# Optimization experiments

Measured on AMD Instinct MI355X. Metric: run time of the kernel, lower is better.

## Reference

```python
import jax, jax.numpy as jnp
import numpy as np

N = 50000   # residue nodes
E = 800000  # edges per edge type
T = 3       # edge types
L = 3       # conv layers (len(hidden_channels)-1)
IN, H, ENC, OUT, K = 64, 128, 100, 32, 128
COMMIT = 0.25
EPS = 1e-5


def gelu(x):
    return jax.nn.gelu(x, approximate=False)  # torch nn.GELU default (erf)


def setup_inputs() -> dict:
    key = jax.random.key(0)
    ks = iter(jax.random.split(key, 40))
    p = lambda shp, s=0.05: jax.random.normal(next(ks), shp, jnp.float32) * s
    inp = {
        'x_res': p((N, IN), 1.0),
        'x_AA': p((N, 20), 1.0),
        'edge_index': jax.random.randint(next(ks), (T, 2, E), 0, N, jnp.int32),
        # input block
        'ln_gamma': jnp.ones((IN,), jnp.float32),
        'ln_beta': jnp.zeros((IN,), jnp.float32),
        'W1': p((IN, 2 * H)), 'b1': jnp.zeros((2 * H,), jnp.float32),
        'W2': p((2 * H, H)), 'b2': jnp.zeros((H,), jnp.float32),
        # body: SAGE convs, [layer, edge_type, ...]
        'sage_Wl': p((L, T, H, H)),  # applied to aggregated neighbors
        'sage_Wr': p((L, T, H, H)),  # applied to root
        'sage_b': jnp.zeros((L, T, H), jnp.float32),
        # GraphNorm per layer
        'gn_weight': jnp.ones((L, H), jnp.float32),
        'gn_bias': jnp.zeros((L, H), jnp.float32),
        'gn_scale': jnp.ones((L, H), jnp.float32),  # mean_scale
        # head
        'Wh1': p((H * L, ENC)), 'bh1': jnp.zeros((ENC,), jnp.float32),
        'Wh2': p((ENC, ENC)), 'bh2': jnp.zeros((ENC,), jnp.float32),
        'Wo1': p((ENC + 20, ENC)), 'bo1': jnp.zeros((ENC,), jnp.float32),
        'Wo2': p((ENC, ENC)), 'bo2': jnp.zeros((ENC,), jnp.float32),
        'Wo3': p((ENC, OUT)), 'bo3': jnp.zeros((OUT,), jnp.float32),
        # VQ codebook
        'codebook': p((K, OUT), 0.5),
    }
    return inp


def _sage(x, src, dst, Wl, Wr, b):
    # SAGEConv, mean aggregation: out = Wl @ mean_{src->dst}(x[src]) + Wr @ x + b
    msg = x[src]                                             # [E, H] gather
    s = jax.ops.segment_sum(msg, dst, num_segments=N)        # [N, H] scatter-add
    cnt = jax.ops.segment_sum(jnp.ones((msg.shape[0],), x.dtype), dst, num_segments=N)
    agg = s / jnp.maximum(cnt, 1.0)[:, None]
    return agg @ Wl + x @ Wr + b


def _graphnorm(x, weight, bias, scale):
    # PyG GraphNorm over a single graph
    out = x - scale * x.mean(0)
    var = (out * out).mean(0)
    return out * jax.lax.rsqrt(var + EPS) * weight + bias


def reference(x_res, x_AA, edge_index, ln_gamma, ln_beta, W1, b1, W2, b2,
              sage_Wl, sage_Wr, sage_b, gn_weight, gn_bias, gn_scale,
              Wh1, bh1, Wh2, bh2, Wo1, bo1, Wo2, bo2, Wo3, bo3, codebook):
    # input: LayerNorm + (dropout = identity in eval) + inmlp
    mu = x_res.mean(-1, keepdims=True)
    var = x_res.var(-1, keepdims=True)
    xr = (x_res - mu) * jax.lax.rsqrt(var + EPS) * ln_gamma + ln_beta
    x = gelu(gelu(xr @ W1 + b1) @ W2 + b2)                   # [N, H]

    # body: per-edge-type SAGE conv -> stack-mean -> GELU -> GraphNorm; JK cat
    x_save = []
    for i in range(L):
        xs = [_sage(x, edge_index[t, 0], edge_index[t, 1],
                    sage_Wl[i, t], sage_Wr[i, t], sage_b[i, t]) for t in range(T)]
        x = jnp.mean(jnp.stack(xs, 0), 0)
        x = gelu(x)
        x = _graphnorm(x, gn_weight[i], gn_bias[i], gn_scale[i])
        x_save.append(x)
    x = jnp.concatenate(x_save, axis=1)                      # [N, H*L] JumpingKnowledge cat

    # head
    x = gelu(gelu(x @ Wh1 + bh1) @ Wh2 + bh2)
    x = jnp.concatenate([x, x_AA], axis=1)
    x = gelu(x @ Wo1 + bo1)
    x = gelu(x @ Wo2 + bo2)
    x = jnp.tanh(x @ Wo3 + bo3)                              # [N, OUT]

    # VectorQuantizer (straight-through)
    d = (jnp.sum(x * x, 1, keepdims=True)
         - 2.0 * x @ codebook.T
         + jnp.sum(codebook * codebook, 1)[None, :])         # [N, K]
    idx = jnp.argmin(d, axis=1)
    q = codebook[idx]                                        # [N, OUT]
    e_latent = jnp.mean((jax.lax.stop_gradient(q) - x) ** 2)
    q_latent = jnp.mean((q - jax.lax.stop_gradient(x)) ** 2)
    vq_loss = q_latent + COMMIT * e_latent
    z_q = x + jax.lax.stop_gradient(q - x)
    return z_q, vq_loss
```

## Files before the change

kernel.cpp:

```cpp
#include <hip/hip_runtime.h>

#define N_ 50000
#define E_ 800000
#define T_ 3
#define NG_ (T_ * N_)
#define EPS_ 1e-5f

__device__ __forceinline__ float gelu_f(float x) {
    return 0.5f * x * (1.0f + erff(x * 0.70710678118654752440f));
}

__global__ void k_prep(const float* __restrict__ Wl, const float* __restrict__ Wr,
                       const float* __restrict__ b, float* wls, float* wra, float* ba) {
    int i = blockIdx.x * 256 + threadIdx.x;
    const float third = 1.0f / 3.0f;
    if (i < 9 * 128 * 128) wls[i] = Wl[i] * third;
    if (i < 3 * 128 * 128) {
        int l = i >> 14, rem = i & 16383;
        const float* p = Wr + l * 3 * 16384 + rem;
        wra[i] = (p[0] + p[16384] + p[32768]) * third;
    }
    if (i < 3 * 128) {
        int l = i >> 7, c = i & 127;
        const float* p = b + l * 3 * 128 + c;
        ba[i] = (p[0] + p[128] + p[256]) * third;
    }
}

__global__ void k_link(const int* __restrict__ EI, int* __restrict__ head, int* __restrict__ nxt) {
    int i = blockIdx.x * 256 + threadIdx.x;
    if (i >= T_ * E_) return;
    int t = i / E_, e = i - t * E_;
    int d = EI[(t * 2 + 1) * E_ + e];
    nxt[i] = atomicExch(&head[t * N_ + d], i);
}

__global__ __launch_bounds__(256) void k_compact(
    const int* __restrict__ EI, const int* __restrict__ head, const int* __restrict__ nxt,
    int* __restrict__ cursor, int* __restrict__ cnt, int* __restrict__ rpA,
    float* __restrict__ inv, int* __restrict__ csr) {
    int tid = threadIdx.x;
    int g = blockIdx.x * 256 + tid;
    bool ok = (g < NG_);
    int lane = tid & 63;
    int c = 0;
    int h = -1;
    if (ok) {
        h = head[g];
        int e = h;
        while (e >= 0) { c++; e = nxt[e]; }
        cnt[g] = c;
        inv[g] = 1.0f / (float)(c > 0 ? c : 1);
    }
    int x = c;
    for (int off = 1; off < 64; off <<= 1) {
        int y = __shfl_up(x, off);
        if (lane >= off) x += y;
    }
    int total = __shfl(x, 63);
    int base = 0;
    if (lane == 63 && total > 0) base = atomicAdd(cursor, total);
    base = __shfl(base, 63);
    if (ok) {
        int pos = base + x - c;
        rpA[g] = pos;
        int e = h;
        while (e >= 0) {
            int t = e / E_, idx = e - t * E_;
            csr[pos++] = EI[(t * 2) * E_ + idx];
            e = nxt[e];
        }
    }
}

__global__ __launch_bounds__(256) void k_inmlp(
    const float* __restrict__ xres, const float* __restrict__ gam, const float* __restrict__ bet,
    const float* __restrict__ W1, const float* __restrict__ b1,
    const float* __restrict__ W2, const float* __restrict__ b2, float* __restrict__ x0) {
    __shared__ float xr[32][68];
    __shared__ float h1[32][260];
    int tid = threadIdx.x;
    int base = blockIdx.x * 32;
    for (int i = 0; i < 2; ++i) {
        int f4 = i * 256 + tid;
        int r = f4 >> 4, c4 = f4 & 15;
        float4 v = make_float4(0.f, 0.f, 0.f, 0.f);
        int gr = base + r;
        if (gr < N_) v = *(const float4*)&xres[gr * 64 + c4 * 4];
        *(float4*)&xr[r][c4 * 4] = v;
    }
    __syncthreads();
    if (tid < 32) {
        int r = tid;
        float s = 0.f;
        for (int k = 0; k < 64; ++k) s += xr[r][k];
        float mu = s * (1.0f / 64.0f);
        float v = 0.f;
        for (int k = 0; k < 64; ++k) { float d = xr[r][k] - mu; v += d * d; }
        float rs = rsqrtf(v * (1.0f / 64.0f) + EPS_);
        for (int k = 0; k < 64; ++k)
            xr[r][k] = (xr[r][k] - mu) * rs * gam[k] + bet[k];
    }
    __syncthreads();
    {
        int tx = tid & 63, ty = tid >> 6;
        int c0 = tx * 4, r0 = ty * 8;
        float acc[8][4];
        for (int r = 0; r < 8; ++r)
            for (int j = 0; j < 4; ++j) acc[r][j] = b1[c0 + j];
        for (int k0 = 0; k0 < 64; k0 += 4) {
            float4 a[8], w[4];
            for (int r = 0; r < 8; ++r) a[r] = *(const float4*)&xr[r0 + r][k0];
            for (int kk = 0; kk < 4; ++kk) w[kk] = *(const float4*)&W1[(k0 + kk) * 256 + c0];
            for (int kk = 0; kk < 4; ++kk)
                for (int r = 0; r < 8; ++r) {
                    float as = (&a[r].x)[kk];
                    acc[r][0] = fmaf(as, w[kk].x, acc[r][0]);
                    acc[r][1] = fmaf(as, w[kk].y, acc[r][1]);
                    acc[r][2] = fmaf(as, w[kk].z, acc[r][2]);
                    acc[r][3] = fmaf(as, w[kk].w, acc[r][3]);
                }
        }
        for (int r = 0; r < 8; ++r)
            for (int j = 0; j < 4; ++j) h1[r0 + r][c0 + j] = gelu_f(acc[r][j]);
    }
    __syncthreads();
    {
        int tx = tid & 31, ty = tid >> 5;
        int c0 = tx * 4, r0 = ty * 4;
        float acc[4][4];
        for (int r = 0; r < 4; ++r)
            for (int j = 0; j < 4; ++j) acc[r][j] = b2[c0 + j];
        for (int k0 = 0; k0 < 256; k0 += 4) {
            float4 a[4], w[4];
            for (int r = 0; r < 4; ++r) a[r] = *(const float4*)&h1[r0 + r][k0];
            for (int kk = 0; kk < 4; ++kk) w[kk] = *(const float4*)&W2[(k0 + kk) * 128 + c0];
            for (int kk = 0; kk < 4; ++kk)
                for (int r = 0; r < 4; ++r) {
                    float as = (&a[r].x)[kk];
                    acc[r][0] = fmaf(as, w[kk].x, acc[r][0]);
                    acc[r][1] = fmaf(as, w[kk].y, acc[r][1]);
                    acc[r][2] = fmaf(as, w[kk].z, acc[r][2]);
                    acc[r][3] = fmaf(as, w[kk].w, acc[r][3]);
                }
        }
        for (int r = 0; r < 4; ++r) {
            int gr = base + r0 + r;
            if (gr < N_) {
                float4 v = make_float4(gelu_f(acc[r][0]), gelu_f(acc[r][1]),
                                       gelu_f(acc[r][2]), gelu_f(acc[r][3]));
                *(float4*)&x0[(long)gr * 128 + c0] = v;
            }
        }
    }
}

__global__ __launch_bounds__(256) void k_gather(
    const int* __restrict__ rpA, const int* __restrict__ cnt, const int* __restrict__ csr,
    const float* __restrict__ inv, const float* __restrict__ X, int ldx, float* __restrict__ agg) {
    int tid = threadIdx.x;
    int g = blockIdx.x * 4 + (tid >> 6);
    if (g >= NG_) return;
    int lane = tid & 63;
    int sub = lane >> 4;
    int f = (lane & 15) * 8;
    int start = rpA[g];
    int end = start + cnt[g];
    float4 s0 = make_float4(0.f, 0.f, 0.f, 0.f);
    float4 s1 = make_float4(0.f, 0.f, 0.f, 0.f);
    for (int e = start + sub; e < end; e += 4) {
        int sn = csr[e];
        const float* row = &X[(long)sn * ldx + f];
        const float4 v0 = *(const float4*)row;
        const float4 v1 = *(const float4*)(row + 4);
        s0.x += v0.x; s0.y += v0.y; s0.z += v0.z; s0.w += v0.w;
        s1.x += v1.x; s1.y += v1.y; s1.z += v1.z; s1.w += v1.w;
    }
    s0.x += __shfl_xor(s0.x, 16); s0.y += __shfl_xor(s0.y, 16);
    s0.z += __shfl_xor(s0.z, 16); s0.w += __shfl_xor(s0.w, 16);
    s1.x += __shfl_xor(s1.x, 16); s1.y += __shfl_xor(s1.y, 16);
    s1.z += __shfl_xor(s1.z, 16); s1.w += __shfl_xor(s1.w, 16);
    s0.x += __shfl_xor(s0.x, 32); s0.y += __shfl_xor(s0.y, 32);
    s0.z += __shfl_xor(s0.z, 32); s0.w += __shfl_xor(s0.w, 32);
    s1.x += __shfl_xor(s1.x, 32); s1.y += __shfl_xor(s1.y, 32);
    s1.z += __shfl_xor(s1.z, 32); s1.w += __shfl_xor(s1.w, 32);
    if (sub == 0) {
        float iv = inv[g];
        float* op = &agg[(long)g * 128 + f];
        *(float4*)op = make_float4(s0.x * iv, s0.y * iv, s0.z * iv, s0.w * iv);
        *(float4*)(op + 4) = make_float4(s1.x * iv, s1.y * iv, s1.z * iv, s1.w * iv);
    }
}

__global__ __launch_bounds__(256) void k_gemm_body(
    const float* __restrict__ X, int ldx, const float* __restrict__ agg,
    const float* __restrict__ wls_l, const float* __restrict__ wra_l, const float* __restrict__ ba_l,
    float* __restrict__ g_out, float* __restrict__ cs_l) {
    __shared__ float xs[64][132];
    __shared__ float sd[8][128];
    int tid = threadIdx.x;
    int base = blockIdx.x * 64;
    int tx = tid & 31, ty = tid >> 5;
    int c0 = tx * 4, r0 = ty * 8;
    float acc[8][4];
    for (int r = 0; r < 8; ++r)
        for (int j = 0; j < 4; ++j) acc[r][j] = ba_l[c0 + j];
    for (int seg = 0; seg < 4; ++seg) {
        const float* src; long ld;
        if (seg < 3) { src = agg + ((long)seg * N_ + base) * 128; ld = 128; }
        else         { src = X + (long)base * ldx; ld = ldx; }
        __syncthreads();
        for (int i = 0; i < 8; ++i) {
            int f4 = i * 256 + tid;
            int r = f4 >> 5, c4 = f4 & 31;
            float4 v = make_float4(0.f, 0.f, 0.f, 0.f);
            if (base + r < N_) v = *(const float4*)&src[(long)r * ld + c4 * 4];
            *(float4*)&xs[r][c4 * 4] = v;
        }
        __syncthreads();
        const float* W = (seg < 3) ? (wls_l + seg * 16384) : wra_l;
        for (int k0 = 0; k0 < 128; k0 += 4) {
            float4 a[8], w[4];
            for (int r = 0; r < 8; ++r) a[r] = *(const float4*)&xs[r0 + r][k0];
            for (int kk = 0; kk < 4; ++kk) w[kk] = *(const float4*)&W[(k0 + kk) * 128 + c0];
            for (int kk = 0; kk < 4; ++kk)
                for (int r = 0; r < 8; ++r) {
                    float as = (&a[r].x)[kk];
                    acc[r][0] = fmaf(as, w[kk].x, acc[r][0]);
                    acc[r][1] = fmaf(as, w[kk].y, acc[r][1]);
                    acc[r][2] = fmaf(as, w[kk].z, acc[r][2]);
                    acc[r][3] = fmaf(as, w[kk].w, acc[r][3]);
                }
        }
    }
    float csum[4] = {0.f, 0.f, 0.f, 0.f};
    for (int r = 0; r < 8; ++r) {
        int gr = base + r0 + r;
        if (gr < N_) {
            float g0 = gelu_f(acc[r][0]), g1 = gelu_f(acc[r][1]);
            float g2 = gelu_f(acc[r][2]), g3 = gelu_f(acc[r][3]);
            *(float4*)&g_out[(long)gr * 128 + c0] = make_float4(g0, g1, g2, g3);
            csum[0] += g0; csum[1] += g1; csum[2] += g2; csum[3] += g3;
        }
    }
    *(float4*)&sd[ty][c0] = make_float4(csum[0], csum[1], csum[2], csum[3]);
    __syncthreads();
    if (tid < 128) {
        float t = 0.f;
        for (int i = 0; i < 8; ++i) t += sd[i][tid];
        atomicAdd(&cs_l[tid], t);
    }
}

__global__ __launch_bounds__(256) void k_pass2(const float* __restrict__ g,
                                               const float* __restrict__ cs_l,
                                               const float* __restrict__ gsc, float* __restrict__ cq_l) {
    __shared__ float sd[256];
    int tid = threadIdx.x;
    int c = tid & 127, half = tid >> 7;
    int base = blockIdx.x * 128 + half * 64;
    float sm = gsc[c] * (cs_l[c] / 50000.0f);
    float s = 0.f;
    for (int i = 0; i < 64; ++i) {
        int r = base + i;
        if (r < N_) { float o = g[(long)r * 128 + c] - sm; s += o * o; }
    }
    sd[tid] = s;
    __syncthreads();
    if (tid < 128) atomicAdd(&cq_l[c], sd[tid] + sd[tid + 128]);
}
__global__ __launch_bounds__(256) void k_pass3(const float* __restrict__ g,
                                               const float* __restrict__ cs_l, const float* __restrict__ cq_l,
                                               const float* __restrict__ gsc,
                                               const float* __restrict__ gw, const float* __restrict__ gb,
                                               float* __restrict__ xs_l) {
    int tid = threadIdx.x;
    int c = tid & 127, half = tid >> 7;
    int base = blockIdx.x * 128 + half * 64;
    float sm = gsc[c] * (cs_l[c] / 50000.0f);
    float var = cq_l[c] / 50000.0f;
    float mul = rsqrtf(var + EPS_) * gw[c];
    float add = gb[c];
    for (int i = 0; i < 64; ++i) {
        int r = base + i;
        if (r < N_) xs_l[(long)r * 384 + c] = (g[(long)r * 128 + c] - sm) * mul + add;
    }
}

__global__ __launch_bounds__(256) void k_head1(const float* __restrict__ xsave,
    const float* __restrict__ Wh1, const float* __restrict__ bh1,
    const float* __restrict__ Wh2, const float* __restrict__ bh2,
    float* __restrict__ h2out) {
    __shared__ float at[64][68];
    __shared__ float h1b[64][104];
    int tid = threadIdx.x;
    int base = blockIdx.x * 64;
    int tx = tid & 31, ty = tid >> 5;
    int c0 = tx * 4, r0 = ty * 8;
    bool valid = (c0 < 100);
    float acc[8][4];
    for (int r = 0; r < 8; ++r)
        for (int j = 0; j < 4; ++j) acc[r][j] = valid ? bh1[c0 + j] : 0.f;
    for (int kt = 0; kt < 6; ++kt) {
        __syncthreads();
        for (int i = 0; i < 4; ++i) {
            int f4 = i * 256 + tid;
            int r = f4 >> 4, c4 = f4 & 15;
            float4 v = make_float4(0.f, 0.f, 0.f, 0.f);
            int gr = base + r;
            if (gr < N_) v = *(const float4*)&xsave[(long)gr * 384 + kt * 64 + c4 * 4];
            *(float4*)&at[r][c4 * 4] = v;
        }
        __syncthreads();
        if (valid) {
            for (int k0 = 0; k0 < 64; k0 += 4) {
                float4 a[8], w[4];
                for (int r = 0; r < 8; ++r) a[r] = *(const float4*)&at[r0 + r][k0];
                for (int kk = 0; kk < 4; ++kk) w[kk] = *(const float4*)&Wh1[(kt * 64 + k0 + kk) * 100 + c0];
                for (int kk = 0; kk < 4; ++kk)
                    for (int r = 0; r < 8; ++r) {
                        float as = (&a[r].x)[kk];
                        acc[r][0] = fmaf(as, w[kk].x, acc[r][0]);
                        acc[r][1] = fmaf(as, w[kk].y, acc[r][1]);
                        acc[r][2] = fmaf(as, w[kk].z, acc[r][2]);
                        acc[r][3] = fmaf(as, w[kk].w, acc[r][3]);
                    }
            }
        }
    }
    __syncthreads();
    if (valid)
        for (int r = 0; r < 8; ++r)
            for (int j = 0; j < 4; ++j) h1b[r0 + r][c0 + j] = gelu_f(acc[r][j]);
    __syncthreads();
    {
        float acc2[8][4];
        for (int r = 0; r < 8; ++r)
            for (int j = 0; j < 4; ++j) acc2[r][j] = valid ? bh2[c0 + j] : 0.f;
        if (valid) {
            for (int k0 = 0; k0 < 100; k0 += 4) {
                float4 a[8], w[4];
                for (int r = 0; r < 8; ++r) a[r] = *(const float4*)&h1b[r0 + r][k0];
                for (int kk = 0; kk < 4; ++kk) w[kk] = *(const float4*)&Wh2[(k0 + kk) * 100 + c0];
                for (int kk = 0; kk < 4; ++kk)
                    for (int r = 0; r < 8; ++r) {
                        float as = (&a[r].x)[kk];
                        acc2[r][0] = fmaf(as, w[kk].x, acc2[r][0]);
                        acc2[r][1] = fmaf(as, w[kk].y, acc2[r][1]);
                        acc2[r][2] = fmaf(as, w[kk].z, acc2[r][2]);
                        acc2[r][3] = fmaf(as, w[kk].w, acc2[r][3]);
                    }
            }
            for (int r = 0; r < 8; ++r) {
                int gr = base + r0 + r;
                if (gr < N_) {
                    float4 v = make_float4(gelu_f(acc2[r][0]), gelu_f(acc2[r][1]),
                                           gelu_f(acc2[r][2]), gelu_f(acc2[r][3]));
                    *(float4*)&h2out[(long)gr * 100 + c0] = v;
                }
            }
        }
    }
}

__global__ __launch_bounds__(128) void k_head2(const float* __restrict__ h2,
    const float* __restrict__ xAA,
    const float* __restrict__ Wo1, const float* __restrict__ bo1,
    const float* __restrict__ Wo2, const float* __restrict__ bo2,
    const float* __restrict__ Wo3, const float* __restrict__ bo3,
    const float* __restrict__ cb, float* __restrict__ zq, float* __restrict__ loss) {
    __shared__ __align__(16) float smem[13216];
    float* A  = smem;
    float* B  = smem + 3968;
    float* XF = smem + 7296;
    float* CB = smem + 8448;
    float* CC = smem + 13056;
    float* SR = smem + 13184;
    int tid = threadIdx.x;
    int base = blockIdx.x * 32;
    for (int i = 0; i < 8; ++i) {
        int f4 = i * 128 + tid;
        int k = f4 >> 3, j4 = f4 & 7;
        float4 v = *(const float4*)&cb[k * 32 + j4 * 4];
        *(float4*)&CB[k * 36 + j4 * 4] = v;
    }
    for (int i = 0; i < 7; ++i) {
        int f4 = i * 128 + tid;
        if (f4 < 800) {
            int r = f4 / 25, c4 = f4 - r * 25;
            float4 v = make_float4(0.f, 0.f, 0.f, 0.f);
            int gr = base + r;
            if (gr < N_) v = *(const float4*)&h2[(long)gr * 100 + c4 * 4];
            *(float4*)&A[r * 124 + c4 * 4] = v;
        }
    }
    for (int i = 0; i < 2; ++i) {
        int f4 = i * 128 + tid;
        if (f4 < 160) {
            int r = f4 / 5, c4 = f4 - r * 5;
            float4 v = make_float4(0.f, 0.f, 0.f, 0.f);
            int gr = base + r;
            if (gr < N_) v = *(const float4*)&xAA[(long)gr * 20 + c4 * 4];
            *(float4*)&A[r * 124 + 100 + c4 * 4] = v;
        }
    }
    __syncthreads();
    if (tid < 128) {
        float s = 0.f;
        for (int j = 0; j < 32; ++j) { float v = CB[tid * 36 + j]; s += v * v; }
        CC[tid] = s;
    }
    int tx = tid & 31, ty = tid >> 5;
    int c0 = tx * 4, r0 = ty * 8;
    bool valid = (c0 < 100);
    {
        float acc[8][4];
        for (int r = 0; r < 8; ++r)
            for (int j = 0; j < 4; ++j) acc[r][j] = valid ? bo1[c0 + j] : 0.f;
        if (valid) {
            for (int k0 = 0; k0 < 120; k0 += 4) {
                float4 a[8], w[4];
                for (int r = 0; r < 8; ++r) a[r] = *(const float4*)&A[(r0 + r) * 124 + k0];
                for (int kk = 0; kk < 4; ++kk) w[kk] = *(const float4*)&Wo1[(k0 + kk) * 100 + c0];
                for (int kk = 0; kk < 4; ++kk)
                    for (int r = 0; r < 8; ++r) {
                        float as = (&a[r].x)[kk];
                        acc[r][0] = fmaf(as, w[kk].x, acc[r][0]);
                        acc[r][1] = fmaf(as, w[kk].y, acc[r][1]);
                        acc[r][2] = fmaf(as, w[kk].z, acc[r][2]);
                        acc[r][3] = fmaf(as, w[kk].w, acc[r][3]);
                    }
            }
        }
        __syncthreads();
        if (valid)
            for (int r = 0; r < 8; ++r)
                for (int j = 0; j < 4; ++j) B[(r0 + r) * 104 + c0 + j] = gelu_f(acc[r][j]);
    }
    __syncthreads();
    {
        float acc[8][4];
        for (int r = 0; r < 8; ++r)
            for (int j = 0; j < 4; ++j) acc[r][j] = valid ? bo2[c0 + j] : 0.f;
        if (valid) {
            for (int k0 = 0; k0 < 100; k0 += 4) {
                float4 a[8], w[4];
                for (int r = 0; r < 8; ++r) a[r] = *(const float4*)&B[(r0 + r) * 104 + k0];
                for (int kk = 0; kk < 4; ++kk) w[kk] = *(const float4*)&Wo2[(k0 + kk) * 100 + c0];
                for (int kk = 0; kk < 4; ++kk)
                    for (int r = 0; r < 8; ++r) {
                        float as = (&a[r].x)[kk];
                        acc[r][0] = fmaf(as, w[kk].x, acc[r][0]);
                        acc[r][1] = fmaf(as, w[kk].y, acc[r][1]);
                        acc[r][2] = fmaf(as, w[kk].z, acc[r][2]);
                        acc[r][3] = fmaf(as, w[kk].w, acc[r][3]);
                    }
            }
        }
        __syncthreads();
        if (valid)
            for (int r = 0; r < 8; ++r)
                for (int j = 0; j < 4; ++j) A[(r0 + r) * 124 + c0 + j] = gelu_f(acc[r][j]);
    }
    __syncthreads();
    {
        int c0b = (tid & 7) * 4, rg = tid >> 3;
        int r0b = rg * 2;
        float acc[2][4];
        for (int r = 0; r < 2; ++r)
            for (int j = 0; j < 4; ++j) acc[r][j] = bo3[c0b + j];
        for (int k0 = 0; k0 < 100; k0 += 4) {
            float4 a[2], w[4];
            for (int r = 0; r < 2; ++r) a[r] = *(const float4*)&A[(r0b + r) * 124 + k0];
            for (int kk = 0; kk < 4; ++kk) w[kk] = *(const float4*)&Wo3[(k0 + kk) * 32 + c0b];
            for (int kk = 0; kk < 4; ++kk)
                for (int r = 0; r < 2; ++r) {
                    float as = (&a[r].x)[kk];
                    acc[r][0] = fmaf(as, w[kk].x, acc[r][0]);
                    acc[r][1] = fmaf(as, w[kk].y, acc[r][1]);
                    acc[r][2] = fmaf(as, w[kk].z, acc[r][2]);
                    acc[r][3] = fmaf(as, w[kk].w, acc[r][3]);
                }
        }
        for (int r = 0; r < 2; ++r)
            for (int j = 0; j < 4; ++j) XF[(r0b + r) * 36 + c0b + j] = tanhf(acc[r][j]);
    }
    __syncthreads();
    {
        int node = tid >> 2, t4 = tid & 3;
        float4 xv[8];
        for (int j4 = 0; j4 < 8; ++j4) xv[j4] = *(const float4*)&XF[node * 36 + j4 * 4];
        float xx = 0.f;
        for (int j4 = 0; j4 < 8; ++j4)
            xx += xv[j4].x * xv[j4].x + xv[j4].y * xv[j4].y + xv[j4].z * xv[j4].z + xv[j4].w * xv[j4].w;
        float best = 3.4e38f;
        int bidx = 0;
        for (int kk = 0; kk < 32; ++kk) {
            int k = kk * 4 + t4;
            const float* cbr = &CB[k * 36];
            float dot = 0.f;
            for (int j4 = 0; j4 < 8; ++j4) {
                float4 cv = *(const float4*)&cbr[j4 * 4];
                dot += cv.x * xv[j4].x + cv.y * xv[j4].y + cv.z * xv[j4].z + cv.w * xv[j4].w;
            }
            float d = fmaf(-2.0f, dot, xx) + CC[k];
            if (d < best) { best = d; bidx = k; }
        }
        for (int off = 1; off < 4; off <<= 1) {
            float ob = __shfl_xor(best, off);
            int oi = __shfl_xor(bidx, off);
            if (ob < best || (ob == best && oi < bidx)) { best = ob; bidx = oi; }
        }
        int gr = base + node;
        if (t4 == 0) {
            float s = 0.f;
            if (gr < N_) {
                const float* q = &CB[bidx * 36];
                for (int j4 = 0; j4 < 8; ++j4) {
                    float4 qv = *(const float4*)&q[j4 * 4];
                    *(float4*)&zq[(long)gr * 32 + j4 * 4] = qv;
                    float4 xvv = xv[j4];
                    float d0 = qv.x - xvv.x, d1 = qv.y - xvv.y, d2 = qv.z - xvv.z, d3 = qv.w - xvv.w;
                    s += d0 * d0 + d1 * d1 + d2 * d2 + d3 * d3;
                }
            }
            SR[node] = s;
        }
    }
    __syncthreads();
    if (tid == 0) {
        float S = 0.f;
        for (int i = 0; i < 32; ++i) S += SR[i];
        atomicAdd(loss, S);
    }
}

__global__ void k_fin(float* dout, const float* loss) {
    if (threadIdx.x == 0 && blockIdx.x == 0)
        dout[(long)N_ * 32] = 1.25f * (loss[0] / 1600000.0f);
}

extern "C" void kernel_launch(void* const* d_in, const int* in_sizes, int n_in,
                              void* d_out, int out_size, void* d_ws, size_t ws_size,
                              hipStream_t stream) {
    const float* x_res = (const float*)d_in[0];
    const float* x_AA  = (const float*)d_in[1];
    const int*   EI    = (const int*)d_in[2];
    const float* ln_g  = (const float*)d_in[3];
    const float* ln_b  = (const float*)d_in[4];
    const float* W1    = (const float*)d_in[5];
    const float* b1    = (const float*)d_in[6];
    const float* W2    = (const float*)d_in[7];
    const float* b2    = (const float*)d_in[8];
    const float* sWl   = (const float*)d_in[9];
    const float* sWr   = (const float*)d_in[10];
    const float* sb    = (const float*)d_in[11];
    const float* gnw   = (const float*)d_in[12];
    const float* gnb   = (const float*)d_in[13];
    const float* gns   = (const float*)d_in[14];
    const float* Wh1   = (const float*)d_in[15];
    const float* bh1   = (const float*)d_in[16];
    const float* Wh2   = (const float*)d_in[17];
    const float* bh2   = (const float*)d_in[18];
    const float* Wo1   = (const float*)d_in[19];
    const float* bo1   = (const float*)d_in[20];
    const float* Wo2   = (const float*)d_in[21];
    const float* bo2   = (const float*)d_in[22];
    const float* Wo3   = (const float*)d_in[23];
    const float* bo3   = (const float*)d_in[24];
    const float* cbk   = (const float*)d_in[25];
    float* out = (float*)d_out;

    float* ws    = (float*)d_ws;
    float* xsave = ws;
    float* x0    = xsave + (size_t)N_ * 384;
    float* agg   = x0 + (size_t)N_ * 128;
    float* gbuf  = agg + (size_t)3 * N_ * 128;
    float* wls   = gbuf + (size_t)N_ * 128;
    float* wra   = wls + 147456;
    float* ba    = wra + 49152;
    int*   cursor = (int*)(ba + 384);
    float* loss  = (float*)(cursor + 1);
    float* cs    = loss + 1;
    float* cq    = cs + 384;
    int*   head  = (int*)(cq + 384);
    int*   nxt   = head + NG_;
    int*   cnt   = nxt + (size_t)T_ * E_;
    int*   rpA   = cnt + NG_;
    float* inv   = (float*)(rpA + NG_);
    int*   csr   = (int*)(inv + NG_);
    float* h2    = agg + (size_t)N_ * 128;

    hipMemsetAsync(cursor, 0, 770 * sizeof(int), stream);
    hipMemsetAsync(head, 0xFF, NG_ * sizeof(int), stream);

    k_prep<<<576, 256, 0, stream>>>(sWl, sWr, sb, wls, wra, ba);
    k_link<<<(T_ * E_ + 255) / 256, 256, 0, stream>>>(EI, head, nxt);
    k_compact<<<(NG_ + 255) / 256, 256, 0, stream>>>(EI, head, nxt, cursor, cnt, rpA, inv, csr);
    k_inmlp<<<(N_ + 31) / 32, 256, 0, stream>>>(x_res, ln_g, ln_b, W1, b1, W2, b2, x0);

    for (int l = 0; l < 3; ++l) {
        const float* X = (l == 0) ? x0 : (xsave + (size_t)(l - 1) * 128);
        int ldx = (l == 0) ? 128 : 384;
        k_gather<<<NG_ / 4, 256, 0, stream>>>(rpA, cnt, csr, inv, X, ldx, agg);
        k_gemm_body<<<(N_ + 63) / 64, 256, 0, stream>>>(X, ldx, agg,
            wls + (size_t)l * 3 * 16384, wra + (size_t)l * 16384, ba + l * 128,
            gbuf, cs + l * 128);
        k_pass2<<<(N_ + 127) / 128, 256, 0, stream>>>(gbuf, cs + l * 128, gns + l * 128, cq + l * 128);
        k_pass3<<<(N_ + 127) / 128, 256, 0, stream>>>(gbuf, cs + l * 128, cq + l * 128,
                                                      gns + l * 128, gnw + l * 128, gnb + l * 128,
                                                      xsave + (size_t)l * 128);
    }
    k_head1<<<(N_ + 63) / 64, 256, 0, stream>>>(xsave, Wh1, bh1, Wh2, bh2, h2);
    k_head2<<<(N_ + 31) / 32, 128, 0, stream>>>(h2, x_AA, Wo1, bo1, Wo2, bo2, Wo3, bo3,
                                                cbk, out, loss);
    k_fin<<<1, 64, 0, stream>>>(out, loss);
}
```

Baseline: 1.549 ms.

## Fuse GraphNorm variance into body GEMM and split head2 into MLP and VQ kernels

The GEMM epilogue now accumulates per-column sums of squares alongside sums, and pass3 derives the GraphNorm variance algebraically from E[g^2], the mean and the mean_scale. This removes the separate pass2 kernel, which re-read the whole gelu output once per layer. The head2 kernel is split into an MLP kernel over 64-row tiles that writes tanh outputs to a workspace buffer, plus a separate VQ kernel with one node per thread that scans all 128 codes. The one-pass variance formula risks cancellation error in fp32, and the split adds an extra global round trip for the 32-wide features.

```diff
diff --git a/kernel.cpp b/kernel.cpp
--- a/kernel.cpp
+++ b/kernel.cpp
@@ -195,9 +195,10 @@
 __global__ __launch_bounds__(256) void k_gemm_body(
     const float* __restrict__ X, int ldx, const float* __restrict__ agg,
     const float* __restrict__ wls_l, const float* __restrict__ wra_l, const float* __restrict__ ba_l,
-    float* __restrict__ g_out, float* __restrict__ cs_l) {
+    float* __restrict__ g_out, float* __restrict__ cs_l, float* __restrict__ cq_l) {
     __shared__ float xs[64][132];
     __shared__ float sd[8][128];
+    __shared__ float sq[8][128];
     int tid = threadIdx.x;
     int base = blockIdx.x * 64;
     int tx = tid & 31, ty = tid >> 5;
@@ -234,6 +235,7 @@
         }
     }
     float csum[4] = {0.f, 0.f, 0.f, 0.f};
+    float qsum[4] = {0.f, 0.f, 0.f, 0.f};
     for (int r = 0; r < 8; ++r) {
         int gr = base + r0 + r;
         if (gr < N_) {
@@ -241,34 +243,20 @@
             float g2 = gelu_f(acc[r][2]), g3 = gelu_f(acc[r][3]);
             *(float4*)&g_out[(long)gr * 128 + c0] = make_float4(g0, g1, g2, g3);
             csum[0] += g0; csum[1] += g1; csum[2] += g2; csum[3] += g3;
+            qsum[0] += g0 * g0; qsum[1] += g1 * g1; qsum[2] += g2 * g2; qsum[3] += g3 * g3;
         }
     }
     *(float4*)&sd[ty][c0] = make_float4(csum[0], csum[1], csum[2], csum[3]);
+    *(float4*)&sq[ty][c0] = make_float4(qsum[0], qsum[1], qsum[2], qsum[3]);
     __syncthreads();
     if (tid < 128) {
-        float t = 0.f;
-        for (int i = 0; i < 8; ++i) t += sd[i][tid];
+        float t = 0.f, q = 0.f;
+        for (int i = 0; i < 8; ++i) { t += sd[i][tid]; q += sq[i][tid]; }
         atomicAdd(&cs_l[tid], t);
-    }
-}
-
-__global__ __launch_bounds__(256) void k_pass2(const float* __restrict__ g,
-                                               const float* __restrict__ cs_l,
-                                               const float* __restrict__ gsc, float* __restrict__ cq_l) {
-    __shared__ float sd[256];
-    int tid = threadIdx.x;
-    int c = tid & 127, half = tid >> 7;
-    int base = blockIdx.x * 128 + half * 64;
-    float sm = gsc[c] * (cs_l[c] / 50000.0f);
-    float s = 0.f;
-    for (int i = 0; i < 64; ++i) {
-        int r = base + i;
-        if (r < N_) { float o = g[(long)r * 128 + c] - sm; s += o * o; }
-    }
-    sd[tid] = s;
-    __syncthreads();
-    if (tid < 128) atomicAdd(&cq_l[c], sd[tid] + sd[tid + 128]);
-}
+        atomicAdd(&cq_l[tid], q);
+    }
+}
+
 __global__ __launch_bounds__(256) void k_pass3(const float* __restrict__ g,
                                                const float* __restrict__ cs_l, const float* __restrict__ cq_l,
                                                const float* __restrict__ gsc,
@@ -277,8 +265,9 @@
     int tid = threadIdx.x;
     int c = tid & 127, half = tid >> 7;
     int base = blockIdx.x * 128 + half * 64;
-    float sm = gsc[c] * (cs_l[c] / 50000.0f);
-    float var = cq_l[c] / 50000.0f;
+    float mu = cs_l[c] / 50000.0f;
+    float sm = gsc[c] * mu;
+    float var = cq_l[c] / 50000.0f - 2.0f * sm * mu + sm * sm;
     float mul = rsqrtf(var + EPS_) * gw[c];
     float add = gb[c];
     for (int i = 0; i < 64; ++i) {
@@ -363,53 +352,37 @@
     }
 }
 
-__global__ __launch_bounds__(128) void k_head2(const float* __restrict__ h2,
+__global__ __launch_bounds__(256) void k_head2a(const float* __restrict__ h2,
     const float* __restrict__ xAA,
     const float* __restrict__ Wo1, const float* __restrict__ bo1,
     const float* __restrict__ Wo2, const float* __restrict__ bo2,
     const float* __restrict__ Wo3, const float* __restrict__ bo3,
-    const float* __restrict__ cb, float* __restrict__ zq, float* __restrict__ loss) {
-    __shared__ __align__(16) float smem[13216];
-    float* A  = smem;
-    float* B  = smem + 3968;
-    float* XF = smem + 7296;
-    float* CB = smem + 8448;
-    float* CC = smem + 13056;
-    float* SR = smem + 13184;
-    int tid = threadIdx.x;
-    int base = blockIdx.x * 32;
-    for (int i = 0; i < 8; ++i) {
-        int f4 = i * 128 + tid;
-        int k = f4 >> 3, j4 = f4 & 7;
-        float4 v = *(const float4*)&cb[k * 32 + j4 * 4];
-        *(float4*)&CB[k * 36 + j4 * 4] = v;
-    }
+    float* __restrict__ xf) {
+    __shared__ float A[64][124];
+    __shared__ float B[64][104];
+    int tid = threadIdx.x;
+    int base = blockIdx.x * 64;
     for (int i = 0; i < 7; ++i) {
-        int f4 = i * 128 + tid;
-        if (f4 < 800) {
+        int f4 = i * 256 + tid;
+        if (f4 < 1600) {
             int r = f4 / 25, c4 = f4 - r * 25;
             float4 v = make_float4(0.f, 0.f, 0.f, 0.f);
             int gr = base + r;
             if (gr < N_) v = *(const float4*)&h2[(long)gr * 100 + c4 * 4];
-            *(float4*)&A[r * 124 + c4 * 4] = v;
+            *(float4*)&A[r][c4 * 4] = v;
         }
     }
     for (int i = 0; i < 2; ++i) {
-        int f4 = i * 128 + tid;
-        if (f4 < 160) {
+        int f4 = i * 256 + tid;
+        if (f4 < 320) {
             int r = f4 / 5, c4 = f4 - r * 5;
             float4 v = make_float4(0.f, 0.f, 0.f, 0.f);
             int gr = base + r;
             if (gr < N_) v = *(const float4*)&xAA[(long)gr * 20 + c4 * 4];
-            *(float4*)&A[r * 124 + 100 + c4 * 4] = v;
-        }
-    }
-    __syncthreads();
-    if (tid < 128) {
-        float s = 0.f;
-        for (int j = 0; j < 32; ++j) { float v = CB[tid * 36 + j]; s += v * v; }
-        CC[tid] = s;
-    }
+            *(float4*)&A[r][100 + c4 * 4] = v;
+        }
+    }
+    __syncthreads();
     int tx = tid & 31, ty = tid >> 5;
     int c0 = tx * 4, r0 = ty * 8;
     bool valid = (c0 < 100);
@@ -420,7 +393,7 @@
         if (valid) {
             for (int k0 = 0; k0 < 120; k0 += 4) {
                 float4 a[8], w[4];
-                for (int r = 0; r < 8; ++r) a[r] = *(const float4*)&A[(r0 + r) * 124 + k0];
+                for (int r = 0; r < 8; ++r) a[r] = *(const float4*)&A[r0 + r][k0];
                 for (int kk = 0; kk < 4; ++kk) w[kk] = *(const float4*)&Wo1[(k0 + kk) * 100 + c0];
                 for (int kk = 0; kk < 4; ++kk)
                     for (int r = 0; r < 8; ++r) {
@@ -431,11 +404,9 @@
                         acc[r][3] = fmaf(as, w[kk].w, acc[r][3]);
                     }
             }
-        }
-        __syncthreads();
-        if (valid)
             for (int r = 0; r < 8; ++r)
-                for (int j = 0; j < 4; ++j) B[(r0 + r) * 104 + c0 + j] = gelu_f(acc[r][j]);
+                for (int j = 0; j < 4; ++j) B[r0 + r][c0 + j] = gelu_f(acc[r][j]);
+        }
     }
     __syncthreads();
     {
@@ -445,7 +416,7 @@
         if (valid) {
             for (int k0 = 0; k0 < 100; k0 += 4) {
                 float4 a[8], w[4];
-                for (int r = 0; r < 8; ++r) a[r] = *(const float4*)&B[(r0 + r) * 104 + k0];
+                for (int r = 0; r < 8; ++r) a[r] = *(const float4*)&B[r0 + r][k0];
                 for (int kk = 0; kk < 4; ++kk) w[kk] = *(const float4*)&Wo2[(k0 + kk) * 100 + c0];
                 for (int kk = 0; kk < 4; ++kk)
                     for (int r = 0; r < 8; ++r) {
@@ -460,7 +431,7 @@
         __syncthreads();
         if (valid)
             for (int r = 0; r < 8; ++r)
-                for (int j = 0; j < 4; ++j) A[(r0 + r) * 124 + c0 + j] = gelu_f(acc[r][j]);
+                for (int j = 0; j < 4; ++j) A[r0 + r][c0 + j] = gelu_f(acc[r][j]);
     }
     __syncthreads();
     {
@@ -471,7 +442,7 @@
             for (int j = 0; j < 4; ++j) acc[r][j] = bo3[c0b + j];
         for (int k0 = 0; k0 < 100; k0 += 4) {
             float4 a[2], w[4];
-            for (int r = 0; r < 2; ++r) a[r] = *(const float4*)&A[(r0b + r) * 124 + k0];
+            for (int r = 0; r < 2; ++r) a[r] = *(const float4*)&A[r0b + r][k0];
             for (int kk = 0; kk < 4; ++kk) w[kk] = *(const float4*)&Wo3[(k0 + kk) * 32 + c0b];
             for (int kk = 0; kk < 4; ++kk)
                 for (int r = 0; r < 2; ++r) {
@@ -482,22 +453,46 @@
                     acc[r][3] = fmaf(as, w[kk].w, acc[r][3]);
                 }
         }
-        for (int r = 0; r < 2; ++r)
-            for (int j = 0; j < 4; ++j) XF[(r0b + r) * 36 + c0b + j] = tanhf(acc[r][j]);
-    }
-    __syncthreads();
-    {
-        int node = tid >> 2, t4 = tid & 3;
+        for (int r = 0; r < 2; ++r) {
+            int gr = base + r0b + r;
+            if (gr < N_) {
+                float4 v = make_float4(tanhf(acc[r][0]), tanhf(acc[r][1]),
+                                       tanhf(acc[r][2]), tanhf(acc[r][3]));
+                *(float4*)&xf[(long)gr * 32 + c0b] = v;
+            }
+        }
+    }
+}
+
+__global__ __launch_bounds__(256) void k_vq(const float* __restrict__ xf,
+    const float* __restrict__ cb, float* __restrict__ zq, float* __restrict__ loss) {
+    __shared__ float CB[128 * 32];
+    __shared__ float CC[128];
+    __shared__ float SR[256];
+    int tid = threadIdx.x;
+    for (int i = 0; i < 4; ++i) {
+        int f4 = i * 256 + tid;
+        *(float4*)&CB[f4 * 4] = *(const float4*)&cb[f4 * 4];
+    }
+    __syncthreads();
+    if (tid < 128) {
+        float s = 0.f;
+        for (int j = 0; j < 32; ++j) { float v = CB[tid * 32 + j]; s += v * v; }
+        CC[tid] = s;
+    }
+    __syncthreads();
+    int node = blockIdx.x * 256 + tid;
+    float part = 0.f;
+    if (node < N_) {
         float4 xv[8];
-        for (int j4 = 0; j4 < 8; ++j4) xv[j4] = *(const float4*)&XF[node * 36 + j4 * 4];
+        for (int j4 = 0; j4 < 8; ++j4) xv[j4] = *(const float4*)&xf[(long)node * 32 + j4 * 4];
         float xx = 0.f;
         for (int j4 = 0; j4 < 8; ++j4)
             xx += xv[j4].x * xv[j4].x + xv[j4].y * xv[j4].y + xv[j4].z * xv[j4].z + xv[j4].w * xv[j4].w;
         float best = 3.4e38f;
         int bidx = 0;
-        for (int kk = 0; kk < 32; ++kk) {
-            int k = kk * 4 + t4;
-            const float* cbr = &CB[k * 36];
+        for (int k = 0; k < 128; ++k) {
+            const float* cbr = &CB[k * 32];
             float dot = 0.f;
             for (int j4 = 0; j4 < 8; ++j4) {
                 float4 cv = *(const float4*)&cbr[j4 * 4];
@@ -506,33 +501,22 @@
             float d = fmaf(-2.0f, dot, xx) + CC[k];
             if (d < best) { best = d; bidx = k; }
         }
-        for (int off = 1; off < 4; off <<= 1) {
-            float ob = __shfl_xor(best, off);
-            int oi = __shfl_xor(bidx, off);
-            if (ob < best || (ob == best && oi < bidx)) { best = ob; bidx = oi; }
-        }
-        int gr = base + node;
-        if (t4 == 0) {
-            float s = 0.f;
-            if (gr < N_) {
-                const float* q = &CB[bidx * 36];
-                for (int j4 = 0; j4 < 8; ++j4) {
-                    float4 qv = *(const float4*)&q[j4 * 4];
-                    *(float4*)&zq[(long)gr * 32 + j4 * 4] = qv;
-                    float4 xvv = xv[j4];
-                    float d0 = qv.x - xvv.x, d1 = qv.y - xvv.y, d2 = qv.z - xvv.z, d3 = qv.w - xvv.w;
-                    s += d0 * d0 + d1 * d1 + d2 * d2 + d3 * d3;
-                }
-            }
-            SR[node] = s;
-        }
-    }
-    __syncthreads();
-    if (tid == 0) {
-        float S = 0.f;
-        for (int i = 0; i < 32; ++i) S += SR[i];
-        atomicAdd(loss, S);
-    }
+        const float* q = &CB[bidx * 32];
+        for (int j4 = 0; j4 < 8; ++j4) {
+            float4 qv = *(const float4*)&q[j4 * 4];
+            *(float4*)&zq[(long)node * 32 + j4 * 4] = qv;
+            float4 xvv = xv[j4];
+            float d0 = qv.x - xvv.x, d1 = qv.y - xvv.y, d2 = qv.z - xvv.z, d3 = qv.w - xvv.w;
+            part += d0 * d0 + d1 * d1 + d2 * d2 + d3 * d3;
+        }
+    }
+    SR[tid] = part;
+    __syncthreads();
+    for (int off = 128; off > 0; off >>= 1) {
+        if (tid < off) SR[tid] += SR[tid + off];
+        __syncthreads();
+    }
+    if (tid == 0) atomicAdd(loss, SR[0]);
 }
 
 __global__ void k_fin(float* dout, const float* loss) {
@@ -590,6 +574,7 @@
     float* inv   = (float*)(rpA + NG_);
     int*   csr   = (int*)(inv + NG_);
     float* h2    = agg + (size_t)N_ * 128;
+    float* xf    = gbuf;
 
     hipMemsetAsync(cursor, 0, 770 * sizeof(int), stream);
     hipMemsetAsync(head, 0xFF, NG_ * sizeof(int), stream);
@@ -605,14 +590,13 @@
         k_gather<<<NG_ / 4, 256, 0, stream>>>(rpA, cnt, csr, inv, X, ldx, agg);
         k_gemm_body<<<(N_ + 63) / 64, 256, 0, stream>>>(X, ldx, agg,
             wls + (size_t)l * 3 * 16384, wra + (size_t)l * 16384, ba + l * 128,
-            gbuf, cs + l * 128);
-        k_pass2<<<(N_ + 127) / 128, 256, 0, stream>>>(gbuf, cs + l * 128, gns + l * 128, cq + l * 128);
+            gbuf, cs + l * 128, cq + l * 128);
         k_pass3<<<(N_ + 127) / 128, 256, 0, stream>>>(gbuf, cs + l * 128, cq + l * 128,
                                                       gns + l * 128, gnw + l * 128, gnb + l * 128,
                                                       xsave + (size_t)l * 128);
     }
     k_head1<<<(N_ + 63) / 64, 256, 0, stream>>>(xsave, Wh1, bh1, Wh2, bh2, h2);
-    k_head2<<<(N_ + 31) / 32, 128, 0, stream>>>(h2, x_AA, Wo1, bo1, Wo2, bo2, Wo3, bo3,
-                                                cbk, out, loss);
+    k_head2a<<<(N_ + 63) / 64, 256, 0, stream>>>(h2, x_AA, Wo1, bo1, Wo2, bo2, Wo3, bo3, xf);
+    k_vq<<<(N_ + 255) / 256, 256, 0, stream>>>(xf, cbk, out, loss);
     k_fin<<<1, 64, 0, stream>>>(out, loss);
 }
```

Result: faster. 1.518 ms (-2.0%).
